# Kernel optimization log

Hardware: AMD Instinct MI355X
Metric: run time of the kernel (lower is better)

Reference implementation:

```python
import jax, jax.numpy as jnp
import numpy as np

B, W, H = 128, 512, 512


def setup_inputs() -> dict:
    key = jax.random.key(0)
    ks = jax.random.split(key, 10)
    s = 1.0 / np.sqrt(H)
    return {
        "g": jax.random.normal(ks[0], (B, H), jnp.float32),
        "c_g": jax.random.normal(ks[1], (B, H), jnp.float32),
        "h": jax.random.normal(ks[2], (B, W, H), jnp.float32),
        "c": jax.random.normal(ks[3], (B, W, H), jnp.float32),
        "W_w": jax.random.normal(ks[4], (2 * H, H), jnp.float32) * s,
        "w_w": jax.random.normal(ks[5], (H, H), jnp.float32) * s,
        "U_w": jax.random.normal(ks[6], (2 * H, H), jnp.float32) * s,
        "U_b": jax.random.normal(ks[7], (2 * H,), jnp.float32) * s,
        "u_w": jax.random.normal(ks[8], (H, H), jnp.float32) * s,
        "u_b": jax.random.normal(ks[9], (H,), jnp.float32) * s,
    }


def reference(g, c_g, h, c, W_w, w_w, U_w, U_b, u_w, u_b):
    hid = w_w.shape[0]
    # attn_pooling: mean over word dim -> [B, H]
    h_avg = jnp.mean(h, axis=-2)
    # gates f, o: [B, H] each
    fo = jax.nn.sigmoid(g @ W_w.T + h_avg @ U_w.T + U_b)
    f, o = fo[..., :hid], fo[..., hid:]
    # per-word forget weights, softmax over word dim: [B, W, H]
    f_w = jax.nn.sigmoid((g @ w_w.T)[..., None, :] + h @ u_w.T + u_b)
    f_w = jax.nn.softmax(f_w, axis=-2)
    new_c = f * c_g + jnp.sum(c * f_w, axis=-2)
    new_g = o * jnp.tanh(new_c)
    return new_g, new_c
```

## Files before the change

### kernel.cpp

```cpp
#include <hip/hip_runtime.h>
#include <stdint.h>

#define BB 128
#define WW 512
#define HH 512
#define TILE 128
#define BK 64

typedef __attribute__((ext_vector_type(8))) short bf16x8;
typedef __attribute__((ext_vector_type(4))) float f32x4;

__device__ __forceinline__ float bf2f(unsigned short u) {
  union { unsigned int i; float f; } v;
  v.i = ((unsigned int)u) << 16;
  return v.f;
}
__device__ __forceinline__ unsigned int pack_bf2(float lo, float hi) {
  union { float f; unsigned int u; } a, b;
  a.f = lo; b.f = hi;
  return (a.u >> 16) | (b.u & 0xFFFF0000u);
}
__device__ __forceinline__ float dot4f(float4 u, const float* gp) {
  return u.x * gp[0] + u.y * gp[1] + u.z * gp[2] + u.w * gp[3];
}
__device__ __forceinline__ void gload_lds16(const void* src, void* lds_dst) {
  __builtin_amdgcn_global_load_lds(
      (const __attribute__((address_space(1))) unsigned int*)src,
      (__attribute__((address_space(3))) unsigned int*)lds_dst, 16, 0, 0);
}

__global__ __launch_bounds__(256) void k01(
    const float* __restrict__ g, const float* __restrict__ W_w,
    const float* __restrict__ w_w, const float* __restrict__ u_w,
    float* __restrict__ gw, float* __restrict__ gfo,
    unsigned short* __restrict__ u_wb) {
  __shared__ __align__(16) unsigned short As[TILE * BK];
  __shared__ __align__(16) unsigned short Bs[TILE * BK];
  const int bid = blockIdx.x;
  const int t = threadIdx.x;

  if (bid >= 12) {
    const int cid0 = (bid - 12) * 256 + t;
    for (int idx = cid0; idx < 32768; idx += 16384) {
      const int kt  = idx >> 12;
      const int rem = idx & 4095;
      const int r   = rem >> 3;
      const int e   = (rem & 7) * 8;
      const int c0  = kt * 64 + (e ^ ((r & 7) << 3));
      const float4* sp = (const float4*)(u_w + (size_t)r * HH + c0);
      float4 s0 = sp[0], s1 = sp[1];
      uint4 pv;
      pv.x = pack_bf2(s0.x, s0.y); pv.y = pack_bf2(s0.z, s0.w);
      pv.z = pack_bf2(s1.x, s1.y); pv.w = pack_bf2(s1.z, s1.w);
      *(uint4*)(u_wb + (size_t)idx * 8) = pv;
    }
    return;
  }

  const int nc = bid;
  const int lane = t & 63, wave = t >> 6;
  const int wm = wave >> 1, wn = wave & 1;
  const int l15 = lane & 15, quad = lane >> 4;

  const float* wsrc = (nc < 4) ? (w_w + (size_t)nc * TILE * HH)
                               : (W_w + (size_t)(nc - 4) * TILE * HH);

  const f32x4 zero = {0.f, 0.f, 0.f, 0.f};
  f32x4 acc[4][4];
#pragma unroll
  for (int i = 0; i < 4; ++i)
#pragma unroll
    for (int j = 0; j < 4; ++j) acc[i][j] = zero;

  const int srow = t >> 3;
  const int scol = (t & 7) * 8;

  for (int kt = 0; kt < 8; ++kt) {
    const int k0 = kt * BK;
#pragma unroll
    for (int p = 0; p < 4; ++p) {
      const int row = p * 32 + srow;
      const float4* ap = (const float4*)(g    + (size_t)row * HH + k0 + scol);
      const float4* bp = (const float4*)(wsrc + (size_t)row * HH + k0 + scol);
      float4 a0 = ap[0], a1 = ap[1], b0 = bp[0], b1 = bp[1];
      uint4 av, bv;
      av.x = pack_bf2(a0.x, a0.y); av.y = pack_bf2(a0.z, a0.w);
      av.z = pack_bf2(a1.x, a1.y); av.w = pack_bf2(a1.z, a1.w);
      bv.x = pack_bf2(b0.x, b0.y); bv.y = pack_bf2(b0.z, b0.w);
      bv.z = pack_bf2(b1.x, b1.y); bv.w = pack_bf2(b1.z, b1.w);
      *(uint4*)(As + row * BK + scol) = av;
      *(uint4*)(Bs + row * BK + scol) = bv;
    }
    __syncthreads();
#pragma unroll
    for (int ks = 0; ks < 2; ++ks) {
      bf16x8 af[4], bg[4];
#pragma unroll
      for (int i = 0; i < 4; ++i)
        af[i] = *(const bf16x8*)(As + (wm * 64 + i * 16 + l15) * BK + ks * 32 + quad * 8);
#pragma unroll
      for (int j = 0; j < 4; ++j)
        bg[j] = *(const bf16x8*)(Bs + (wn * 64 + j * 16 + l15) * BK + ks * 32 + quad * 8);
#pragma unroll
      for (int i = 0; i < 4; ++i)
#pragma unroll
        for (int j = 0; j < 4; ++j)
          acc[i][j] = __builtin_amdgcn_mfma_f32_16x16x32_bf16(af[i], bg[j], acc[i][j], 0, 0, 0);
    }
    __syncthreads();
  }

#pragma unroll
  for (int j = 0; j < 4; ++j) {
    const int nl = wn * 64 + j * 16 + l15;
#pragma unroll
    for (int i = 0; i < 4; ++i) {
#pragma unroll
      for (int r = 0; r < 4; ++r) {
        const int b = wm * 64 + i * 16 + quad * 4 + r;
        const float v = acc[i][j][r];
        if (nc < 4) gw[(size_t)b * HH + nc * TILE + nl] = v;
        else        gfo[(size_t)b * 2 * HH + (nc - 4) * TILE + nl] = v;
      }
    }
  }
}

__global__ __launch_bounds__(512, 2) void k2_fused(
    const float* __restrict__ h, const float* __restrict__ c,
    const unsigned short* __restrict__ u_wb, const float* __restrict__ u_b,
    const float* __restrict__ gw,
    float* __restrict__ hsumP, float* __restrict__ denP, float* __restrict__ numP) {
  __shared__ __align__(16) unsigned short Bs[512 * 64];
  __shared__ __align__(16) unsigned short As[128 * 64];
  __shared__ float colred[8][64];
  __shared__ float redD[2][512];
  __shared__ float redN[2][512];

  const int bid = blockIdx.x;
  const int b = bid >> 2, wc = bid & 3;
  const int t = threadIdx.x;
  const int lane = t & 63, wave = t >> 6;
  const int wm = wave >> 2, wn = wave & 3;
  const int l15 = lane & 15, quad = lane >> 4;

  const size_t hbase = ((size_t)b * WW + (size_t)wc * 128) * HH;

  const f32x4 zero = {0.f, 0.f, 0.f, 0.f};
  f32x4 acc[4][8];
#pragma unroll
  for (int i = 0; i < 4; ++i)
#pragma unroll
    for (int j = 0; j < 8; ++j) acc[i][j] = zero;

  const int srow = t >> 3;
  const int scol = (t & 7) * 8;

  for (int kt = 0; kt < 8; ++kt) {
    const int k0 = kt * 64;

    if (kt > 0 && t < 64) {
      float tot = 0.f;
#pragma unroll
      for (int gq = 0; gq < 8; ++gq) tot += colred[gq][t];
      hsumP[((size_t)b * 4 + wc) * HH + (kt - 1) * 64 + t] = tot;
    }

#pragma unroll
    for (int it = 0; it < 8; ++it) {
      const int s = wave * 8 + it;
      const unsigned short* src =
          u_wb + ((size_t)kt * 32768 + (size_t)s * 512 + (size_t)lane * 8);
      gload_lds16(src, Bs + (size_t)s * 512);
    }

#pragma unroll
    for (int p = 0; p < 2; ++p) {
      const int row = p * 64 + srow;
      const float4* ap = (const float4*)(h + hbase + (size_t)row * HH + k0 + scol);
      float4 a0 = ap[0], a1 = ap[1];
      uint4 av;
      av.x = pack_bf2(a0.x, a0.y); av.y = pack_bf2(a0.z, a0.w);
      av.z = pack_bf2(a1.x, a1.y); av.w = pack_bf2(a1.z, a1.w);
      *(uint4*)(As + row * 64 + (scol ^ ((row & 7) << 3))) = av;
    }
    __syncthreads();

    {
      const int col = t & 63, gq = t >> 6;
      float s = 0.f;
#pragma unroll
      for (int rr = 0; rr < 16; ++rr) {
        const int row = gq * 16 + rr;
        s += bf2f(As[row * 64 + (col ^ ((row & 7) << 3))]);
      }
      colred[gq][col] = s;
    }

#pragma unroll
    for (int ks = 0; ks < 2; ++ks) {
      bf16x8 af[4], bg[8];
#pragma unroll
      for (int i = 0; i < 4; ++i) {
        const int row = wm * 64 + i * 16 + l15;
        af[i] = *(const bf16x8*)(As + row * 64 + ((ks * 32 + quad * 8) ^ ((row & 7) << 3)));
      }
#pragma unroll
      for (int j = 0; j < 8; ++j) {
        const int row = wn * 128 + j * 16 + l15;
        bg[j] = *(const bf16x8*)(Bs + row * 64 + ((ks * 32 + quad * 8) ^ ((row & 7) << 3)));
      }
#pragma unroll
      for (int i = 0; i < 4; ++i)
#pragma unroll
        for (int j = 0; j < 8; ++j)
          acc[i][j] = __builtin_amdgcn_mfma_f32_16x16x32_bf16(af[i], bg[j], acc[i][j], 0, 0, 0);
    }
    __syncthreads();
  }

  if (t < 64) {
    float tot = 0.f;
#pragma unroll
    for (int gq = 0; gq < 8; ++gq) tot += colred[gq][t];
    hsumP[((size_t)b * 4 + wc) * HH + 7 * 64 + t] = tot;
  }

#pragma unroll
  for (int j = 0; j < 8; ++j) {
    const int n = wn * 128 + j * 16 + l15;
    const float gwub = gw[(size_t)b * HH + n] + u_b[n];
    float dsum = 0.f, nsum = 0.f;
#pragma unroll
    for (int i = 0; i < 4; ++i) {
#pragma unroll
      for (int r = 0; r < 4; ++r) {
        const int m = wm * 64 + i * 16 + quad * 4 + r;
        const float z = acc[i][j][r] + gwub;
        const float sig = 1.f / (1.f + __expf(-z));
        const float e = __expf(sig);
        dsum += e;
        nsum += e * c[hbase + (size_t)m * HH + n];
      }
    }
    dsum += __shfl_xor(dsum, 16);
    dsum += __shfl_xor(dsum, 32);
    nsum += __shfl_xor(nsum, 16);
    nsum += __shfl_xor(nsum, 32);
    if (quad == 0) { redD[wm][n] = dsum; redN[wm][n] = nsum; }
  }
  __syncthreads();
  {
    const size_t o = ((size_t)b * 4 + wc) * HH + t;
    denP[o] = redD[0][t] + redD[1][t];
    numP[o] = redN[0][t] + redN[1][t];
  }
}

__global__ __launch_bounds__(256) void k3_final(
    const float* __restrict__ c_g, const float* __restrict__ U_w,
    const float* __restrict__ U_b,
    const float* __restrict__ gfo, const float* __restrict__ hsumP,
    const float* __restrict__ denP, const float* __restrict__ numP,
    float* __restrict__ out) {
  __shared__ __align__(16) float ha[HH];
  __shared__ float ncL[128];
  __shared__ float oL[128];
  const int bid = blockIdx.x;
  const int b = bid >> 2, q = bid & 3;
  const int t = threadIdx.x;

  for (int i = t; i < HH; i += 256) {
    const float* hp = hsumP + (size_t)b * 4 * HH + i;
    ha[i] = (hp[0] + hp[HH] + hp[2 * HH] + hp[3 * HH]) * (1.f / (float)WW);
  }
  __syncthreads();

  const int isF = (t < 128);
  const int n = q * 128 + (t & 127);
  const int row = isF ? n : (HH + n);
  const float4* up = (const float4*)(U_w + (size_t)row * HH);

  float p0 = 0.f, p1 = 0.f, p2 = 0.f, p3 = 0.f;
#pragma unroll 4
  for (int k4 = 0; k4 < 128; k4 += 4) {
    p0 += dot4f(up[k4 + 0], ha + k4 * 4 + 0);
    p1 += dot4f(up[k4 + 1], ha + k4 * 4 + 4);
    p2 += dot4f(up[k4 + 2], ha + k4 * 4 + 8);
    p3 += dot4f(up[k4 + 3], ha + k4 * 4 + 12);
  }
  const float dot = (p0 + p1) + (p2 + p3);
  const float logit = gfo[(size_t)b * 2 * HH + row] + dot + U_b[row];
  const float sg = 1.f / (1.f + __expf(-logit));

  if (isF) {
    const float* dp = denP + (size_t)b * 4 * HH + n;
    const float* np = numP + (size_t)b * 4 * HH + n;
    const float den = dp[0] + dp[HH] + dp[2 * HH] + dp[3 * HH];
    const float num = np[0] + np[HH] + np[2 * HH] + np[3 * HH];
    const float ncv = sg * c_g[(size_t)b * HH + n] + num / den;
    ncL[t] = ncv;
    out[(size_t)BB * HH + (size_t)b * HH + n] = ncv;
  } else {
    oL[t - 128] = sg;
  }
  __syncthreads();
  if (isF) {
    out[(size_t)b * HH + n] = oL[t] * tanhf(ncL[t]);
  }
}

extern "C" void kernel_launch(void* const* d_in, const int* in_sizes, int n_in,
                              void* d_out, int out_size, void* d_ws, size_t ws_size,
                              hipStream_t stream) {
  const float* g   = (const float*)d_in[0];
  const float* c_g = (const float*)d_in[1];
  const float* h   = (const float*)d_in[2];
  const float* c   = (const float*)d_in[3];
  const float* W_w = (const float*)d_in[4];
  const float* w_w = (const float*)d_in[5];
  const float* U_w = (const float*)d_in[6];
  const float* U_b = (const float*)d_in[7];
  const float* u_w = (const float*)d_in[8];
  const float* u_b = (const float*)d_in[9];

  float* ws    = (float*)d_ws;
  float* gw    = ws;
  float* gfo   = gw + BB * HH;
  float* hsumP = gfo + (size_t)BB * 2 * HH;
  float* denP  = hsumP + (size_t)BB * 4 * HH;
  float* numP  = denP + (size_t)BB * 4 * HH;
  unsigned short* u_wb = (unsigned short*)(numP + (size_t)BB * 4 * HH);
  float* out = (float*)d_out;

  hipLaunchKernelGGL(k01, dim3(76), dim3(256), 0, stream, g, W_w, w_w, u_w, gw, gfo, u_wb);
  hipLaunchKernelGGL(k2_fused, dim3(512), dim3(512), 0, stream,
                     h, c, u_wb, u_b, gw, hsumP, denP, numP);
  hipLaunchKernelGGL(k3_final, dim3(512), dim3(256), 0, stream,
                     c_g, U_w, U_b, gfo, hsumP, denP, numP, out);
}
```

Baseline: 372.1 us.

## Split fused gate GEMM across N halves and coalesce final U_w dot products

The main fused kernel now splits the 512-wide hidden output into two 256-column halves, one per block. This doubles the grid to 1024 blocks, halves LDS and accumulator size, and raises the occupancy hint to 4 blocks per CU. The cost is that each h tile is loaded and converted to bf16 twice. The u_w bf16 pre-pack layout is reordered so each half's tiles are contiguous, and only half 0 computes the column sums of h. The final kernel replaces per-thread strided row dot products with wave-per-row coalesced loads reduced by shuffles.

```diff
diff --git a/kernel.cpp b/kernel.cpp
--- a/kernel.cpp
+++ b/kernel.cpp
@@ -20,8 +20,8 @@
   a.f = lo; b.f = hi;
   return (a.u >> 16) | (b.u & 0xFFFF0000u);
 }
-__device__ __forceinline__ float dot4f(float4 u, const float* gp) {
-  return u.x * gp[0] + u.y * gp[1] + u.z * gp[2] + u.w * gp[3];
+__device__ __forceinline__ float dot4v(float4 u, float4 v) {
+  return u.x * v.x + u.y * v.y + u.z * v.z + u.w * v.w;
 }
 __device__ __forceinline__ void gload_lds16(const void* src, void* lds_dst) {
   __builtin_amdgcn_global_load_lds(
@@ -42,12 +42,14 @@
   if (bid >= 12) {
     const int cid0 = (bid - 12) * 256 + t;
     for (int idx = cid0; idx < 32768; idx += 16384) {
-      const int kt  = idx >> 12;
-      const int rem = idx & 4095;
-      const int r   = rem >> 3;
-      const int e   = (rem & 7) * 8;
-      const int c0  = kt * 64 + (e ^ ((r & 7) << 3));
-      const float4* sp = (const float4*)(u_w + (size_t)r * HH + c0);
+      const int tile = idx >> 11;
+      const int rem  = idx & 2047;
+      const int row  = rem >> 3;
+      const int eg   = (rem & 7) * 8;
+      const int nh   = tile >> 3;
+      const int kt   = tile & 7;
+      const int c0   = kt * 64 + (eg ^ ((row & 7) << 3));
+      const float4* sp = (const float4*)(u_w + (size_t)(nh * 256 + row) * HH + c0);
       float4 s0 = sp[0], s1 = sp[1];
       uint4 pv;
       pv.x = pack_bf2(s0.x, s0.y); pv.y = pack_bf2(s0.z, s0.w);
@@ -126,32 +128,35 @@
   }
 }
 
-__global__ __launch_bounds__(512, 2) void k2_fused(
+__global__ __launch_bounds__(512, 4) void k2_fused(
     const float* __restrict__ h, const float* __restrict__ c,
     const unsigned short* __restrict__ u_wb, const float* __restrict__ u_b,
     const float* __restrict__ gw,
     float* __restrict__ hsumP, float* __restrict__ denP, float* __restrict__ numP) {
-  __shared__ __align__(16) unsigned short Bs[512 * 64];
+  __shared__ __align__(16) unsigned short Bs[256 * 64];
   __shared__ __align__(16) unsigned short As[128 * 64];
   __shared__ float colred[8][64];
-  __shared__ float redD[2][512];
-  __shared__ float redN[2][512];
+  __shared__ float redD[2][256];
+  __shared__ float redN[2][256];
 
   const int bid = blockIdx.x;
-  const int b = bid >> 2, wc = bid & 3;
+  const int b  = bid >> 3;
+  const int wc = (bid >> 1) & 3;
+  const int nh = bid & 1;
   const int t = threadIdx.x;
   const int lane = t & 63, wave = t >> 6;
   const int wm = wave >> 2, wn = wave & 3;
   const int l15 = lane & 15, quad = lane >> 4;
 
   const size_t hbase = ((size_t)b * WW + (size_t)wc * 128) * HH;
+  const unsigned short* ubase = u_wb + (size_t)nh * 8 * 16384;
 
   const f32x4 zero = {0.f, 0.f, 0.f, 0.f};
-  f32x4 acc[4][8];
+  f32x4 acc[4][4];
 #pragma unroll
   for (int i = 0; i < 4; ++i)
 #pragma unroll
-    for (int j = 0; j < 8; ++j) acc[i][j] = zero;
+    for (int j = 0; j < 4; ++j) acc[i][j] = zero;
 
   const int srow = t >> 3;
   const int scol = (t & 7) * 8;
@@ -159,7 +164,7 @@
   for (int kt = 0; kt < 8; ++kt) {
     const int k0 = kt * 64;
 
-    if (kt > 0 && t < 64) {
+    if (nh == 0 && kt > 0 && t < 64) {
       float tot = 0.f;
 #pragma unroll
       for (int gq = 0; gq < 8; ++gq) tot += colred[gq][t];
@@ -167,10 +172,10 @@
     }
 
 #pragma unroll
-    for (int it = 0; it < 8; ++it) {
-      const int s = wave * 8 + it;
+    for (int it = 0; it < 4; ++it) {
+      const int s = wave * 4 + it;
       const unsigned short* src =
-          u_wb + ((size_t)kt * 32768 + (size_t)s * 512 + (size_t)lane * 8);
+          ubase + ((size_t)kt * 16384 + (size_t)s * 512 + (size_t)lane * 8);
       gload_lds16(src, Bs + (size_t)s * 512);
     }
 
@@ -186,7 +191,7 @@
     }
     __syncthreads();
 
-    {
+    if (nh == 0) {
       const int col = t & 63, gq = t >> 6;
       float s = 0.f;
 #pragma unroll
@@ -199,37 +204,38 @@
 
 #pragma unroll
     for (int ks = 0; ks < 2; ++ks) {
-      bf16x8 af[4], bg[8];
+      bf16x8 af[4], bg[4];
 #pragma unroll
       for (int i = 0; i < 4; ++i) {
         const int row = wm * 64 + i * 16 + l15;
         af[i] = *(const bf16x8*)(As + row * 64 + ((ks * 32 + quad * 8) ^ ((row & 7) << 3)));
       }
 #pragma unroll
-      for (int j = 0; j < 8; ++j) {
-        const int row = wn * 128 + j * 16 + l15;
+      for (int j = 0; j < 4; ++j) {
+        const int row = wn * 64 + j * 16 + l15;
         bg[j] = *(const bf16x8*)(Bs + row * 64 + ((ks * 32 + quad * 8) ^ ((row & 7) << 3)));
       }
 #pragma unroll
       for (int i = 0; i < 4; ++i)
 #pragma unroll
-        for (int j = 0; j < 8; ++j)
+        for (int j = 0; j < 4; ++j)
           acc[i][j] = __builtin_amdgcn_mfma_f32_16x16x32_bf16(af[i], bg[j], acc[i][j], 0, 0, 0);
     }
     __syncthreads();
   }
 
-  if (t < 64) {
+  if (nh == 0 && t < 64) {
     float tot = 0.f;
 #pragma unroll
     for (int gq = 0; gq < 8; ++gq) tot += colred[gq][t];
     hsumP[((size_t)b * 4 + wc) * HH + 7 * 64 + t] = tot;
   }
 
-#pragma unroll
-  for (int j = 0; j < 8; ++j) {
-    const int n = wn * 128 + j * 16 + l15;
-    const float gwub = gw[(size_t)b * HH + n] + u_b[n];
+  const int N0 = nh * 256;
+#pragma unroll
+  for (int j = 0; j < 4; ++j) {
+    const int n = wn * 64 + j * 16 + l15;
+    const float gwub = gw[(size_t)b * HH + N0 + n] + u_b[N0 + n];
     float dsum = 0.f, nsum = 0.f;
 #pragma unroll
     for (int i = 0; i < 4; ++i) {
@@ -240,7 +246,7 @@
         const float sig = 1.f / (1.f + __expf(-z));
         const float e = __expf(sig);
         dsum += e;
-        nsum += e * c[hbase + (size_t)m * HH + n];
+        nsum += e * c[hbase + (size_t)m * HH + N0 + n];
       }
     }
     dsum += __shfl_xor(dsum, 16);
@@ -250,8 +256,8 @@
     if (quad == 0) { redD[wm][n] = dsum; redN[wm][n] = nsum; }
   }
   __syncthreads();
-  {
-    const size_t o = ((size_t)b * 4 + wc) * HH + t;
+  if (t < 256) {
+    const size_t o = ((size_t)b * 4 + wc) * HH + N0 + t;
     denP[o] = redD[0][t] + redD[1][t];
     numP[o] = redN[0][t] + redN[1][t];
   }
@@ -263,34 +269,50 @@
     const float* __restrict__ gfo, const float* __restrict__ hsumP,
     const float* __restrict__ denP, const float* __restrict__ numP,
     float* __restrict__ out) {
-  __shared__ __align__(16) float ha[HH];
+  __shared__ float logitL[256];
   __shared__ float ncL[128];
   __shared__ float oL[128];
   const int bid = blockIdx.x;
   const int b = bid >> 2, q = bid & 3;
   const int t = threadIdx.x;
-
-  for (int i = t; i < HH; i += 256) {
-    const float* hp = hsumP + (size_t)b * 4 * HH + i;
-    ha[i] = (hp[0] + hp[HH] + hp[2 * HH] + hp[3 * HH]) * (1.f / (float)WW);
+  const int lane = t & 63, wave = t >> 6;
+
+  float4 ha0 = {0.f, 0.f, 0.f, 0.f}, ha1 = {0.f, 0.f, 0.f, 0.f};
+  {
+    const float4* hp = (const float4*)(hsumP + (size_t)b * 4 * HH);
+#pragma unroll
+    for (int p = 0; p < 4; ++p) {
+      float4 a = hp[p * 128 + lane * 2];
+      float4 bq = hp[p * 128 + lane * 2 + 1];
+      ha0.x += a.x; ha0.y += a.y; ha0.z += a.z; ha0.w += a.w;
+      ha1.x += bq.x; ha1.y += bq.y; ha1.z += bq.z; ha1.w += bq.w;
+    }
+    const float sc = 1.f / (float)WW;
+    ha0.x *= sc; ha0.y *= sc; ha0.z *= sc; ha0.w *= sc;
+    ha1.x *= sc; ha1.y *= sc; ha1.z *= sc; ha1.w *= sc;
+  }
+
+#pragma unroll 2
+  for (int r = 0; r < 64; ++r) {
+    const int idx = wave * 64 + r;
+    const int urow = (idx < 128) ? (q * 128 + idx) : (HH + q * 128 + (idx - 128));
+    const float4* up = (const float4*)(U_w + (size_t)urow * HH);
+    float4 u0 = up[lane * 2], u1 = up[lane * 2 + 1];
+    float s = dot4v(u0, ha0) + dot4v(u1, ha1);
+    s += __shfl_xor(s, 1);
+    s += __shfl_xor(s, 2);
+    s += __shfl_xor(s, 4);
+    s += __shfl_xor(s, 8);
+    s += __shfl_xor(s, 16);
+    s += __shfl_xor(s, 32);
+    if (lane == 0) logitL[idx] = s;
   }
   __syncthreads();
 
   const int isF = (t < 128);
   const int n = q * 128 + (t & 127);
   const int row = isF ? n : (HH + n);
-  const float4* up = (const float4*)(U_w + (size_t)row * HH);
-
-  float p0 = 0.f, p1 = 0.f, p2 = 0.f, p3 = 0.f;
-#pragma unroll 4
-  for (int k4 = 0; k4 < 128; k4 += 4) {
-    p0 += dot4f(up[k4 + 0], ha + k4 * 4 + 0);
-    p1 += dot4f(up[k4 + 1], ha + k4 * 4 + 4);
-    p2 += dot4f(up[k4 + 2], ha + k4 * 4 + 8);
-    p3 += dot4f(up[k4 + 3], ha + k4 * 4 + 12);
-  }
-  const float dot = (p0 + p1) + (p2 + p3);
-  const float logit = gfo[(size_t)b * 2 * HH + row] + dot + U_b[row];
+  const float logit = logitL[t] + gfo[(size_t)b * 2 * HH + row] + U_b[row];
   const float sg = 1.f / (1.f + __expf(-logit));
 
   if (isF) {
@@ -334,7 +356,7 @@
   float* out = (float*)d_out;
 
   hipLaunchKernelGGL(k01, dim3(76), dim3(256), 0, stream, g, W_w, w_w, u_w, gw, gfo, u_wb);
-  hipLaunchKernelGGL(k2_fused, dim3(512), dim3(512), 0, stream,
+  hipLaunchKernelGGL(k2_fused, dim3(1024), dim3(512), 0, stream,
                      h, c, u_wb, u_b, gw, hsumP, denP, numP);
   hipLaunchKernelGGL(k3_final, dim3(512), dim3(256), 0, stream,
                      c_g, U_w, U_b, gfo, hsumP, denP, numP, out);
```

Result: slower. 383.0 us (+2.9%).
